# Kernel tuning notes

Measured on AMD Instinct MI355X. Metric: run time of the kernel, lower is better.

The kernel has to match this reference:

```python
import jax, jax.numpy as jnp
import numpy as np

B, S, D = 2, 2048, 512
H = 8
HD = D // H  # head dim = 64


def setup_inputs() -> dict:
    key = jax.random.key(0)
    ks = jax.random.split(key, 4)
    scale = 1.0 / np.sqrt(D)
    x = jax.random.normal(ks[0], (B, S, D), dtype=jnp.float32)
    wq = jax.random.normal(ks[1], (D, D), dtype=jnp.float32) * scale
    wk = jax.random.normal(ks[2], (D, D), dtype=jnp.float32) * scale
    wv = jax.random.normal(ks[3], (D, D), dtype=jnp.float32) * scale
    bq = jnp.zeros((D,), dtype=jnp.float32)
    bk = jnp.zeros((D,), dtype=jnp.float32)
    bv = jnp.zeros((D,), dtype=jnp.float32)
    return {"x": x, "wq": wq, "bq": bq, "wk": wk, "bk": bk, "wv": wv, "bv": bv}


def reference(x, wq, bq, wk, bk, wv, bv):
    # Linear projections (torch Linear: y = x @ W^T + b; weights here stored as [out,in])
    q = x @ wq.T + bq  # [B,S,D]
    k = x @ wk.T + bk
    v = x @ wv.T + bv
    # split heads -> [B,H,S,HD]
    q = q.reshape(B, S, H, HD).transpose(0, 2, 1, 3)
    k = k.reshape(B, S, H, HD).transpose(0, 2, 1, 3)
    v = v.reshape(B, S, H, HD).transpose(0, 2, 1, 3)
    # QK^T scores, scaled by 1/sqrt(head_dim)
    scores = jnp.einsum("bhqd,bhkd->bhqk", q, k) / jnp.sqrt(jnp.float32(HD))
    # softmax-free: elementwise sigmoid instead of softmax normalization
    attn = jax.nn.sigmoid(scores)  # [B,H,S,S] — the memory-bound intermediate
    out = jnp.einsum("bhqk,bhkd->bhqd", attn, v)
    # merge heads -> [B,S,D]
    return out.transpose(0, 2, 1, 3).reshape(B, S, D)
```

## Files before the change

kernel.cpp:

```cpp
#include <hip/hip_runtime.h>
#include <cstdint>
#include <cstddef>

#define BB   2
#define SS   2048
#define DD   512
#define HH   8
#define HDIM 64

typedef __attribute__((ext_vector_type(8)))  short          s16x8;
typedef __attribute__((ext_vector_type(16))) float          f32x16;

static __device__ __forceinline__ unsigned short f2bf(float f) {
  union { float f; unsigned u; } x; x.f = f;
  unsigned r = x.u + 0x7fffu + ((x.u >> 16) & 1u);
  return (unsigned short)(r >> 16);
}
static __device__ __forceinline__ unsigned packtrunc(float lo, float hi) {
  return __builtin_amdgcn_perm(__float_as_uint(hi), __float_as_uint(lo), 0x07060302u);
}

#define QSCALE (-0.18033688011111543f)

__global__ __launch_bounds__(256) void proj_kernel(
    const float* __restrict__ x,
    const float* __restrict__ wq, const float* __restrict__ wk, const float* __restrict__ wv,
    const float* __restrict__ bq, const float* __restrict__ bk, const float* __restrict__ bv,
    unsigned short* __restrict__ qo, unsigned short* __restrict__ ko,
    unsigned short* __restrict__ vt) {
  __shared__ unsigned short As[2][64 * 40];
  __shared__ unsigned short Bs[2][64 * 40];

  const int z = blockIdx.z;
  const float* w; const float* bias;
  if (z == 0)      { w = wq; bias = bq; }
  else if (z == 1) { w = wk; bias = bk; }
  else             { w = wv; bias = bv; }

  const int t = threadIdx.x;
  const int lane = t & 63, wave = t >> 6;
  const int ln = lane & 31, hi = lane >> 5;
  const int wr = wave >> 1, wc = wave & 1;
  const int m0 = blockIdx.x * 64, n0 = blockIdx.y * 64;

  float4 ar[2], br[2];
#pragma unroll
  for (int i = 0; i < 2; i++) {
    int c = t + i * 256;
    ar[i] = *(const float4*)&x[(size_t)(m0 + (c >> 3)) * DD + (c & 7) * 4];
    br[i] = *(const float4*)&w[(size_t)(n0 + (c >> 3)) * DD + (c & 7) * 4];
  }
#pragma unroll
  for (int i = 0; i < 2; i++) {
    int c = t + i * 256;
    uint2 ua, ub;
    ua.x = packtrunc(ar[i].x, ar[i].y); ua.y = packtrunc(ar[i].z, ar[i].w);
    ub.x = packtrunc(br[i].x, br[i].y); ub.y = packtrunc(br[i].z, br[i].w);
    *(uint2*)&As[0][(c >> 3) * 40 + (c & 7) * 4] = ua;
    *(uint2*)&Bs[0][(c >> 3) * 40 + (c & 7) * 4] = ub;
  }
  __syncthreads();

  f32x16 acc = {};

#pragma unroll 2
  for (int kt = 0; kt < 16; kt++) {
    const int cur = kt & 1, nxt = cur ^ 1;
    if (kt < 15) {
      int k0 = (kt + 1) * 32;
#pragma unroll
      for (int i = 0; i < 2; i++) {
        int c = t + i * 256;
        ar[i] = *(const float4*)&x[(size_t)(m0 + (c >> 3)) * DD + k0 + (c & 7) * 4];
        br[i] = *(const float4*)&w[(size_t)(n0 + (c >> 3)) * DD + k0 + (c & 7) * 4];
      }
    }
#pragma unroll
    for (int c = 0; c < 2; c++) {
      s16x8 af = *(const s16x8*)&As[cur][(wr * 32 + ln) * 40 + c * 16 + hi * 8];
      s16x8 bf = *(const s16x8*)&Bs[cur][(wc * 32 + ln) * 40 + c * 16 + hi * 8];
      acc = __builtin_amdgcn_mfma_f32_32x32x16_bf16(af, bf, acc, 0, 0, 0);
    }
    if (kt < 15) {
#pragma unroll
      for (int i = 0; i < 2; i++) {
        int c = t + i * 256;
        uint2 ua, ub;
        ua.x = packtrunc(ar[i].x, ar[i].y); ua.y = packtrunc(ar[i].z, ar[i].w);
        ub.x = packtrunc(br[i].x, br[i].y); ub.y = packtrunc(br[i].z, br[i].w);
        *(uint2*)&As[nxt][(c >> 3) * 40 + (c & 7) * 4] = ua;
        *(uint2*)&Bs[nxt][(c >> 3) * 40 + (c & 7) * 4] = ub;
      }
    }
    __syncthreads();
  }

  const int h = blockIdx.y;
  const int bidx = m0 >> 11;
  const int sbase = (m0 & 2047) + wr * 32;
  const int hd = wc * 32 + ln;
  const float bval = bias[n0 + hd];
  const size_t bhb = (size_t)(bidx * HH + h) * SS * HDIM;

  if (z == 0) {
#pragma unroll
    for (int r = 0; r < 16; r++) {
      int s = sbase + (r & 3) + 8 * (r >> 2) + 4 * hi;
      qo[bhb + (size_t)s * HDIM + hd] = f2bf((acc[r] + bval) * QSCALE);
    }
  } else if (z == 1) {
    const int c = hd >> 4, hk = (hd >> 3) & 1, j = hd & 7;
    const int kts = sbase >> 5;
    unsigned short* kd = ko + bhb + ((size_t)kts * 4 + c) * 512 + j;
#pragma unroll
    for (int r = 0; r < 16; r++) {
      int off = (r & 3) + 8 * (r >> 2) + 4 * hi;
      kd[(hk * 32 + off) * 8] = f2bf(acc[r] + bval);
    }
  } else {
    const int kts = sbase >> 5;
    unsigned short* vd = vt + bhb + ((size_t)kts * 4 + wc * 2) * 512 + hi * 256 + ln * 8;
#pragma unroll
    for (int g = 0; g < 4; g++) {
      unsigned short* vg = vd + (g >> 1) * 512 + (g & 1) * 4;
#pragma unroll
      for (int j = 0; j < 4; j += 2) {
        unsigned pk = (unsigned)f2bf(acc[g * 4 + j] + bval) |
                      ((unsigned)f2bf(acc[g * 4 + j + 1] + bval) << 16);
        *(unsigned*)&vg[j] = pk;
      }
    }
  }
}

__global__ __launch_bounds__(512, 4) void attn_kernel(
    const unsigned short* __restrict__ qb,
    const unsigned short* __restrict__ kfb,
    const unsigned short* __restrict__ vfb,
    float* __restrict__ out) {
  __shared__ __align__(16) float red[2 * 4096];

  const int t = threadIdx.x;
  const int lane = t & 63, wave = t >> 6;
  const int ln = lane & 31, hi = lane >> 5;
  const int qh = wave & 1, kh = wave >> 1;
  const int fid = blockIdx.y * 32 + blockIdx.x;
  const int bh = fid & 15, qx = fid >> 4;
  const int b = bh >> 3, h = bh & 7;
  const unsigned short* qp = qb + (size_t)bh * SS * HDIM;
  const unsigned short* kfp = kfb + (size_t)bh * SS * HDIM;
  const unsigned short* vfp = vfb + (size_t)bh * SS * HDIM;
  const int q0 = qx * 64;

  s16x8 qf[4];
#pragma unroll
  for (int c = 0; c < 4; c++)
    qf[c] = *(const s16x8*)&qp[(size_t)(q0 + qh * 32 + ln) * HDIM + c * 16 + hi * 8];

  f32x16 o0 = {}, o1 = {};

  s16x8 kf[4], vf[4];
  int foff = kh * 16 * 2048 + lane * 8;
#pragma unroll
  for (int c = 0; c < 4; c++) {
    kf[c] = *(const s16x8*)&kfp[foff + c * 512];
    vf[c] = *(const s16x8*)&vfp[foff + c * 512];
  }
  foff += 2048;

#pragma unroll 1
  for (int i = 0; i < 16; i++) {
    f32x16 st = {};
#pragma unroll
    for (int c = 0; c < 4; c++)
      st = __builtin_amdgcn_mfma_f32_32x32x16_bf16(kf[c], qf[c], st, 0, 0, 0);

    if (i < 15) {
#pragma unroll
      for (int c = 0; c < 4; c++)
        kf[c] = *(const s16x8*)&kfp[foff + c * 512];
    }

    unsigned pg[8];
#pragma unroll
    for (int g = 0; g < 4; g++) {
      float p0 = __builtin_amdgcn_rcpf(1.0f + __builtin_amdgcn_exp2f(st[4 * g + 0]));
      float p1 = __builtin_amdgcn_rcpf(1.0f + __builtin_amdgcn_exp2f(st[4 * g + 1]));
      float p2 = __builtin_amdgcn_rcpf(1.0f + __builtin_amdgcn_exp2f(st[4 * g + 2]));
      float p3 = __builtin_amdgcn_rcpf(1.0f + __builtin_amdgcn_exp2f(st[4 * g + 3]));
      pg[2 * g]     = packtrunc(p0, p1);
      pg[2 * g + 1] = packtrunc(p2, p3);
    }

#pragma unroll
    for (int c = 0; c < 2; c++) {
      union { unsigned u[4]; s16x8 v; } pu;
      pu.u[0] = pg[4 * c + 0];
      pu.u[1] = pg[4 * c + 1];
      pu.u[2] = pg[4 * c + 2];
      pu.u[3] = pg[4 * c + 3];
      o0 = __builtin_amdgcn_mfma_f32_32x32x16_bf16(pu.v, vf[c], o0, 0, 0, 0);
      o1 = __builtin_amdgcn_mfma_f32_32x32x16_bf16(pu.v, vf[2 + c], o1, 0, 0, 0);
    }

    if (i < 15) {
#pragma unroll
      for (int c = 0; c < 4; c++)
        vf[c] = *(const s16x8*)&vfp[foff + c * 512];
      foff += 2048;
    }
  }

  if (kh >= 2) {
    const int slot = kh - 2;
#pragma unroll
    for (int dh = 0; dh < 2; dh++) {
      f32x16 ov = dh ? o1 : o0;
#pragma unroll
      for (int r = 0; r < 16; r++) {
        int ql = (r & 3) + 8 * (r >> 2) + 4 * hi;
        red[slot * 4096 + (qh * 32 + ql) * 64 + dh * 32 + ln] = ov[r];
      }
    }
  }
  __syncthreads();
  if (kh < 2) {
#pragma unroll
    for (int dh = 0; dh < 2; dh++) {
      f32x16 ov = dh ? o1 : o0;
#pragma unroll
      for (int r = 0; r < 16; r++) {
        int ql = (r & 3) + 8 * (r >> 2) + 4 * hi;
        red[kh * 4096 + (qh * 32 + ql) * 64 + dh * 32 + ln] += ov[r];
      }
    }
  }
  __syncthreads();
  const float4* r0 = (const float4*)red;
  const float4* r1 = (const float4*)(red + 4096);
#pragma unroll
  for (int j = 0; j < 2; j++) {
    int g = t + j * 512;
    float4 s0 = r0[g], s1 = r1[g];
    float4 s;
    s.x = s0.x + s1.x; s.y = s0.y + s1.y; s.z = s0.z + s1.z; s.w = s0.w + s1.w;
    int q = g >> 4, dbase = (g & 15) * 4;
    *(float4*)&out[((size_t)(b * SS + q0 + q)) * DD + h * HDIM + dbase] = s;
  }
}

extern "C" void kernel_launch(void* const* d_in, const int* in_sizes, int n_in,
                              void* d_out, int out_size, void* d_ws, size_t ws_size,
                              hipStream_t stream) {
  const float* x  = (const float*)d_in[0];
  const float* wq = (const float*)d_in[1];
  const float* bq = (const float*)d_in[2];
  const float* wk = (const float*)d_in[3];
  const float* bk = (const float*)d_in[4];
  const float* wv = (const float*)d_in[5];
  const float* bv = (const float*)d_in[6];
  float* out = (float*)d_out;

  constexpr size_t XN = (size_t)BB * SS * DD;

  unsigned short* qo = (unsigned short*)d_ws;
  unsigned short* ko = qo + XN;
  unsigned short* vt = ko + XN;

  proj_kernel<<<dim3(64, 8, 3), 256, 0, stream>>>(x, wq, wk, wv, bq, bk, bv, qo, ko, vt);
  attn_kernel<<<dim3(SS / 64, BB * HH), 512, 0, stream>>>(qo, ko, vt, out);
}
```

Baseline: 114.5 us.

## Pre-convert inputs to bf16 in a separate pass and enlarge projection M tile

Adds a conversion kernel that casts x and the three weight matrices to bf16 once. The projection kernel then loads bf16 directly instead of fp32 with in-kernel packing, so the redundant fp32 reads and conversions across the many blocks that share each x row and weight tile go away. The projection tile grows from 64 to 128 rows, with each wave computing two 32x32 MFMA outputs. The cost is an extra kernel launch and an extra round trip of about 8 MB through global memory. Rounding also changes from truncation to round-to-nearest.

```diff
diff --git a/kernel.cpp b/kernel.cpp
--- a/kernel.cpp
+++ b/kernel.cpp
@@ -7,8 +7,11 @@
 #define DD   512
 #define HH   8
 #define HDIM 64
+#define XN   ((size_t)BB * SS * DD)
+#define WN   ((size_t)DD * DD)
 
 typedef __attribute__((ext_vector_type(8)))  short          s16x8;
+typedef __attribute__((ext_vector_type(8)))  unsigned short u16x8;
 typedef __attribute__((ext_vector_type(16))) float          f32x16;
 
 static __device__ __forceinline__ unsigned short f2bf(float f) {
@@ -22,46 +25,58 @@
 
 #define QSCALE (-0.18033688011111543f)
 
-__global__ __launch_bounds__(256) void proj_kernel(
+__global__ __launch_bounds__(256) void cvt_kernel(
     const float* __restrict__ x,
     const float* __restrict__ wq, const float* __restrict__ wk, const float* __restrict__ wv,
+    unsigned short* __restrict__ xb, unsigned short* __restrict__ wb3) {
+  const int y = blockIdx.y;
+  const float* src; unsigned short* dst;
+  if (y == 0) { src = x; dst = xb; }
+  else {
+    if (blockIdx.x >= 256) return;
+    src = (y == 1) ? wq : (y == 2) ? wk : wv;
+    dst = wb3 + (size_t)(y - 1) * WN;
+  }
+  int i = (blockIdx.x * 256 + threadIdx.x) * 4;
+  float4 f = *(const float4*)(src + i);
+  ushort4 o;
+  o.x = f2bf(f.x); o.y = f2bf(f.y); o.z = f2bf(f.z); o.w = f2bf(f.w);
+  *(ushort4*)(dst + i) = o;
+}
+
+__global__ __launch_bounds__(256) void proj_kernel(
+    const unsigned short* __restrict__ xb, const unsigned short* __restrict__ wb3,
     const float* __restrict__ bq, const float* __restrict__ bk, const float* __restrict__ bv,
     unsigned short* __restrict__ qo, unsigned short* __restrict__ ko,
     unsigned short* __restrict__ vt) {
-  __shared__ unsigned short As[2][64 * 40];
+  __shared__ unsigned short As[2][128 * 40];
   __shared__ unsigned short Bs[2][64 * 40];
 
   const int z = blockIdx.z;
-  const float* w; const float* bias;
-  if (z == 0)      { w = wq; bias = bq; }
-  else if (z == 1) { w = wk; bias = bk; }
-  else             { w = wv; bias = bv; }
+  const unsigned short* w = wb3 + (size_t)z * WN;
+  const float* bias = (z == 0) ? bq : (z == 1) ? bk : bv;
 
   const int t = threadIdx.x;
   const int lane = t & 63, wave = t >> 6;
   const int ln = lane & 31, hi = lane >> 5;
-  const int wr = wave >> 1, wc = wave & 1;
-  const int m0 = blockIdx.x * 64, n0 = blockIdx.y * 64;
-
-  float4 ar[2], br[2];
+  const int m0 = blockIdx.x * 128, n0 = blockIdx.y * 64;
+
+  u16x8 ar[2], br;
 #pragma unroll
   for (int i = 0; i < 2; i++) {
     int c = t + i * 256;
-    ar[i] = *(const float4*)&x[(size_t)(m0 + (c >> 3)) * DD + (c & 7) * 4];
-    br[i] = *(const float4*)&w[(size_t)(n0 + (c >> 3)) * DD + (c & 7) * 4];
-  }
+    ar[i] = *(const u16x8*)&xb[(size_t)(m0 + (c >> 2)) * DD + (c & 3) * 8];
+  }
+  br = *(const u16x8*)&w[(size_t)(n0 + (t >> 2)) * DD + (t & 3) * 8];
 #pragma unroll
   for (int i = 0; i < 2; i++) {
     int c = t + i * 256;
-    uint2 ua, ub;
-    ua.x = packtrunc(ar[i].x, ar[i].y); ua.y = packtrunc(ar[i].z, ar[i].w);
-    ub.x = packtrunc(br[i].x, br[i].y); ub.y = packtrunc(br[i].z, br[i].w);
-    *(uint2*)&As[0][(c >> 3) * 40 + (c & 7) * 4] = ua;
-    *(uint2*)&Bs[0][(c >> 3) * 40 + (c & 7) * 4] = ub;
-  }
+    *(u16x8*)&As[0][(c >> 2) * 40 + (c & 3) * 8] = ar[i];
+  }
+  *(u16x8*)&Bs[0][(t >> 2) * 40 + (t & 3) * 8] = br;
   __syncthreads();
 
-  f32x16 acc = {};
+  f32x16 acc0 = {}, acc1 = {};
 
 #pragma unroll 2
   for (int kt = 0; kt < 16; kt++) {
@@ -71,63 +86,66 @@
 #pragma unroll
       for (int i = 0; i < 2; i++) {
         int c = t + i * 256;
-        ar[i] = *(const float4*)&x[(size_t)(m0 + (c >> 3)) * DD + k0 + (c & 7) * 4];
-        br[i] = *(const float4*)&w[(size_t)(n0 + (c >> 3)) * DD + k0 + (c & 7) * 4];
-      }
-    }
-#pragma unroll
-    for (int c = 0; c < 2; c++) {
-      s16x8 af = *(const s16x8*)&As[cur][(wr * 32 + ln) * 40 + c * 16 + hi * 8];
-      s16x8 bf = *(const s16x8*)&Bs[cur][(wc * 32 + ln) * 40 + c * 16 + hi * 8];
-      acc = __builtin_amdgcn_mfma_f32_32x32x16_bf16(af, bf, acc, 0, 0, 0);
+        ar[i] = *(const u16x8*)&xb[(size_t)(m0 + (c >> 2)) * DD + k0 + (c & 3) * 8];
+      }
+      br = *(const u16x8*)&w[(size_t)(n0 + (t >> 2)) * DD + k0 + (t & 3) * 8];
+    }
+#pragma unroll
+    for (int cc = 0; cc < 2; cc++) {
+      s16x8 af = *(const s16x8*)&As[cur][(wave * 32 + ln) * 40 + cc * 16 + hi * 8];
+      s16x8 b0 = *(const s16x8*)&Bs[cur][(ln) * 40 + cc * 16 + hi * 8];
+      s16x8 b1 = *(const s16x8*)&Bs[cur][(32 + ln) * 40 + cc * 16 + hi * 8];
+      acc0 = __builtin_amdgcn_mfma_f32_32x32x16_bf16(af, b0, acc0, 0, 0, 0);
+      acc1 = __builtin_amdgcn_mfma_f32_32x32x16_bf16(af, b1, acc1, 0, 0, 0);
     }
     if (kt < 15) {
 #pragma unroll
       for (int i = 0; i < 2; i++) {
         int c = t + i * 256;
-        uint2 ua, ub;
-        ua.x = packtrunc(ar[i].x, ar[i].y); ua.y = packtrunc(ar[i].z, ar[i].w);
-        ub.x = packtrunc(br[i].x, br[i].y); ub.y = packtrunc(br[i].z, br[i].w);
-        *(uint2*)&As[nxt][(c >> 3) * 40 + (c & 7) * 4] = ua;
-        *(uint2*)&Bs[nxt][(c >> 3) * 40 + (c & 7) * 4] = ub;
-      }
+        *(u16x8*)&As[nxt][(c >> 2) * 40 + (c & 3) * 8] = ar[i];
+      }
+      *(u16x8*)&Bs[nxt][(t >> 2) * 40 + (t & 3) * 8] = br;
     }
     __syncthreads();
   }
 
   const int h = blockIdx.y;
   const int bidx = m0 >> 11;
-  const int sbase = (m0 & 2047) + wr * 32;
-  const int hd = wc * 32 + ln;
-  const float bval = bias[n0 + hd];
+  const int sbase = (m0 & 2047) + wave * 32;
   const size_t bhb = (size_t)(bidx * HH + h) * SS * HDIM;
-
-  if (z == 0) {
-#pragma unroll
-    for (int r = 0; r < 16; r++) {
-      int s = sbase + (r & 3) + 8 * (r >> 2) + 4 * hi;
-      qo[bhb + (size_t)s * HDIM + hd] = f2bf((acc[r] + bval) * QSCALE);
-    }
-  } else if (z == 1) {
-    const int c = hd >> 4, hk = (hd >> 3) & 1, j = hd & 7;
-    const int kts = sbase >> 5;
-    unsigned short* kd = ko + bhb + ((size_t)kts * 4 + c) * 512 + j;
-#pragma unroll
-    for (int r = 0; r < 16; r++) {
-      int off = (r & 3) + 8 * (r >> 2) + 4 * hi;
-      kd[(hk * 32 + off) * 8] = f2bf(acc[r] + bval);
-    }
-  } else {
-    const int kts = sbase >> 5;
-    unsigned short* vd = vt + bhb + ((size_t)kts * 4 + wc * 2) * 512 + hi * 256 + ln * 8;
-#pragma unroll
-    for (int g = 0; g < 4; g++) {
-      unsigned short* vg = vd + (g >> 1) * 512 + (g & 1) * 4;
-#pragma unroll
-      for (int j = 0; j < 4; j += 2) {
-        unsigned pk = (unsigned)f2bf(acc[g * 4 + j] + bval) |
-                      ((unsigned)f2bf(acc[g * 4 + j + 1] + bval) << 16);
-        *(unsigned*)&vg[j] = pk;
+  const int kts = sbase >> 5;
+
+#pragma unroll
+  for (int nh = 0; nh < 2; nh++) {
+    f32x16 acc = nh ? acc1 : acc0;
+    const int hd = nh * 32 + ln;
+    const float bval = bias[n0 + hd];
+
+    if (z == 0) {
+#pragma unroll
+      for (int r = 0; r < 16; r++) {
+        int s = sbase + (r & 3) + 8 * (r >> 2) + 4 * hi;
+        qo[bhb + (size_t)s * HDIM + hd] = f2bf((acc[r] + bval) * QSCALE);
+      }
+    } else if (z == 1) {
+      const int c = hd >> 4, hk = (hd >> 3) & 1, j = hd & 7;
+      unsigned short* kd = ko + bhb + ((size_t)kts * 4 + c) * 512 + j;
+#pragma unroll
+      for (int r = 0; r < 16; r++) {
+        int off = (r & 3) + 8 * (r >> 2) + 4 * hi;
+        kd[(hk * 32 + off) * 8] = f2bf(acc[r] + bval);
+      }
+    } else {
+      unsigned short* vd = vt + bhb + ((size_t)kts * 4 + nh * 2) * 512 + hi * 256 + ln * 8;
+#pragma unroll
+      for (int g = 0; g < 4; g++) {
+        unsigned short* vg = vd + (g >> 1) * 512 + (g & 1) * 4;
+#pragma unroll
+        for (int j = 0; j < 4; j += 2) {
+          unsigned pk = (unsigned)f2bf(acc[g * 4 + j] + bval) |
+                        ((unsigned)f2bf(acc[g * 4 + j + 1] + bval) << 16);
+          *(unsigned*)&vg[j] = pk;
+        }
       }
     }
   }
@@ -261,12 +279,13 @@
   const float* bv = (const float*)d_in[6];
   float* out = (float*)d_out;
 
-  constexpr size_t XN = (size_t)BB * SS * DD;
-
-  unsigned short* qo = (unsigned short*)d_ws;
+  unsigned short* xb = (unsigned short*)d_ws;
+  unsigned short* wb = xb + XN;
+  unsigned short* qo = wb + 3 * WN;
   unsigned short* ko = qo + XN;
   unsigned short* vt = ko + XN;
 
-  proj_kernel<<<dim3(64, 8, 3), 256, 0, stream>>>(x, wq, wk, wv, bq, bk, bv, qo, ko, vt);
+  cvt_kernel<<<dim3(2048, 4), 256, 0, stream>>>(x, wq, wk, wv, xb, wb);
+  proj_kernel<<<dim3(32, 8, 3), 256, 0, stream>>>(xb, wb, bq, bk, bv, qo, ko, vt);
   attn_kernel<<<dim3(SS / 64, BB * HH), 512, 0, stream>>>(qo, ko, vt, out);
 }
```

New measurement: 113.5 us. No clear change (-0.9%).
